# Kernel tuning notes

Measured on AMD Instinct MI355X. Metric: run time of the kernel, lower is better.

## Reference

```python
import jax, jax.numpy as jnp
import numpy as np

N_NODES = 50000
N_EDGES = 800000
DIM = 128
HEADS = 2
DEPTH = 2
MLP = 512
NEG_SLOPE = 0.2  # PyG GATv2 default
EPS = 1e-5


def setup_inputs() -> dict:
    key = jax.random.key(0)
    ks = jax.random.split(key, 10)
    s = 0.05
    p = lambda k, shape: (jax.random.normal(k, shape, jnp.float32) * s)
    x = jax.random.normal(ks[0], (N_NODES, DIM), jnp.float32)
    edge_index = jax.random.randint(ks[1], (2, N_EDGES), 0, N_NODES, dtype=jnp.int64)
    D, H = DEPTH, HEADS
    return {
        "x": x,
        "edge_index": edge_index,
        # per-layer stacked params (leading dim = depth)
        "ln1_g": jnp.ones((D, DIM), jnp.float32), "ln1_b": jnp.zeros((D, DIM), jnp.float32),
        "Wl": p(ks[2], (D, DIM, H * DIM)), "bl": jnp.zeros((D, H * DIM), jnp.float32),
        "Wr": p(ks[3], (D, DIM, H * DIM)), "br": jnp.zeros((D, H * DIM), jnp.float32),
        "att": p(ks[4], (D, H, DIM)),
        "gat_b": jnp.zeros((D, H * DIM), jnp.float32),
        "proj_W": p(ks[5], (D, H * DIM, DIM)), "proj_b": jnp.zeros((D, DIM), jnp.float32),
        "ln2_g": jnp.ones((D, DIM), jnp.float32), "ln2_b": jnp.zeros((D, DIM), jnp.float32),
        "W1": p(ks[6], (D, DIM, MLP)), "b1": jnp.zeros((D, MLP), jnp.float32),
        "W2": p(ks[7], (D, MLP, DIM)), "b2": jnp.zeros((D, DIM), jnp.float32),
    }


def _layer_norm(x, g, b):
    m = jnp.mean(x, axis=-1, keepdims=True)
    v = jnp.var(x, axis=-1, keepdims=True)
    return (x - m) * jax.lax.rsqrt(v + EPS) * g + b


def _gatv2(x, src, dst, Wl, bl, Wr, br, att, gat_b):
    # GATv2Conv: e_ij = att^T LeakyReLU(Wl x_j + Wr x_i); alpha = segment-softmax over dst
    n = x.shape[0]
    xl = (x @ Wl + bl).reshape(n, HEADS, DIM)  # source transform [N,H,D]
    xr = (x @ Wr + br).reshape(n, HEADS, DIM)  # target transform [N,H,D]
    e = jax.nn.leaky_relu(xl[src] + xr[dst], NEG_SLOPE)      # [E,H,D]
    score = jnp.einsum('ehd,hd->eh', e, att)                 # [E,H]
    smax = jax.ops.segment_max(score, dst, num_segments=n)   # [N,H]
    ex = jnp.exp(score - smax[dst])
    denom = jax.ops.segment_sum(ex, dst, num_segments=n)     # [N,H]
    alpha = ex / (denom[dst] + 1e-16)                        # [E,H]
    msg = xl[src] * alpha[..., None]                         # [E,H,D]
    out = jax.ops.segment_sum(msg, dst, num_segments=n)      # [N,H,D]
    return out.reshape(n, HEADS * DIM) + gat_b


def reference(x, edge_index, ln1_g, ln1_b, Wl, bl, Wr, br, att, gat_b,
              proj_W, proj_b, ln2_g, ln2_b, W1, b1, W2, b2):
    src, dst = edge_index[0], edge_index[1]
    for i in range(DEPTH):
        h = _layer_norm(x, ln1_g[i], ln1_b[i])               # PreNorm
        g = _gatv2(h, src, dst, Wl[i], bl[i], Wr[i], br[i], att[i], gat_b[i])
        x = x + (g @ proj_W[i] + proj_b[i])                  # QuickFix proj + Residual
        h = _layer_norm(x, ln2_g[i], ln2_b[i])
        x = x + (jax.nn.gelu(h @ W1[i] + b1[i]) @ W2[i] + b2[i])  # FFN + Residual
    return x
```

## Files before the change

kernel.cpp:

```cpp
#include <hip/hip_runtime.h>

typedef unsigned int uint;
typedef unsigned short ushort;
typedef __attribute__((ext_vector_type(4))) float f32x4;
typedef __attribute__((ext_vector_type(2))) float f32x2;
typedef __attribute__((ext_vector_type(8))) short bf16x8;
typedef _Float16 f16x2 __attribute__((ext_vector_type(2)));

#define N_NODES 50000
#define DIM 128
#define HEADS 2
#define HD 256
#define MLP 512
#define DEPTH 2
#define CAP 96
#define NPART 8
#define BPX 104

__device__ __forceinline__ uint f2bf(float f) {
    uint u = __float_as_uint(f);
    return (u + 0x7FFFu + ((u >> 16) & 1u)) >> 16;
}
__device__ __forceinline__ ushort f2h(float f) {
    union { _Float16 h; ushort u; } v;
    v.h = (_Float16)f;
    return v.u;
}
__device__ __forceinline__ f16x2 u2h(uint u) {
    union { uint u; f16x2 h; } v;
    v.u = u;
    return v.h;
}

#if __has_builtin(__builtin_amdgcn_fdot2)
#define FDOT2(a, b, c) __builtin_amdgcn_fdot2((a), (b), (c), false)
#else
#define FDOT2(a, b, c) fmaf((float)(a)[0], (float)(b)[0], fmaf((float)(a)[1], (float)(b)[1], (c)))
#endif
#if __has_builtin(__builtin_amdgcn_exp2f)
#define EXP2F(x) __builtin_amdgcn_exp2f(x)
#else
#define EXP2F(x) exp2f(x)
#endif

__device__ __forceinline__ float gelu_tanh(float x) {
    float t = 0.7978845608028654f * (x + 0.044715f * x * x * x);
    float e = __expf(2.0f * t);
    float th = 1.0f - 2.0f / (e + 1.0f);
    return 0.5f * x * (1.0f + th);
}

__global__ __launch_bounds__(256) void ln_kernel(
    const float* __restrict__ x, const float* __restrict__ g,
    const float* __restrict__ b, ushort* __restrict__ out, int N)
{
    int node = blockIdx.x * 4 + (threadIdx.x >> 6);
    if (node >= N) return;
    int lane = threadIdx.x & 63;
    const float2 v = *(const float2*)(x + (size_t)node * DIM + lane * 2);
    float s = v.x + v.y;
    float s2 = v.x * v.x + v.y * v.y;
    #pragma unroll
    for (int m = 1; m <= 32; m <<= 1) {
        s  += __shfl_xor(s,  m, 64);
        s2 += __shfl_xor(s2, m, 64);
    }
    float mean = s * (1.0f / 128.0f);
    float var  = s2 * (1.0f / 128.0f) - mean * mean;
    float rs = rsqrtf(var + 1e-5f);
    float ox = (v.x - mean) * rs * g[lane * 2]     + b[lane * 2];
    float oy = (v.y - mean) * rs * g[lane * 2 + 1] + b[lane * 2 + 1];
    uint pk = f2bf(ox) | (f2bf(oy) << 16);
    *(uint*)(out + (size_t)node * DIM + lane * 2) = pk;
}

__global__ __launch_bounds__(256) void wconv_all(
    const float* __restrict__ Wl, const float* __restrict__ Wr,
    const float* __restrict__ pW, const float* __restrict__ W1,
    const float* __restrict__ W2, ushort* __restrict__ WlWr_t,
    ushort* __restrict__ pW_t, ushort* __restrict__ W1_t,
    ushort* __restrict__ W2_t)
{
    int i = blockIdx.x * 256 + threadIdx.x;
    if (i < 65536) {
        int l = i >> 15, rem = i & 32767;
        int k = rem >> 8, m = rem & 255;
        WlWr_t[l * 65536 + m * 128 + k] = (ushort)f2bf(Wl[i]);
    } else if (i < 131072) {
        int j = i - 65536;
        int l = j >> 15, rem = j & 32767;
        int k = rem >> 8, m = rem & 255;
        WlWr_t[l * 65536 + (m + 256) * 128 + k] = (ushort)f2bf(Wr[j]);
    } else if (i < 196608) {
        int j = i - 131072;
        int l = j >> 15, rem = j & 32767;
        int k = rem >> 7, m = rem & 127;
        pW_t[l * 32768 + m * 256 + k] = (ushort)f2bf(pW[j]);
    } else if (i < 327680) {
        int j = i - 196608;
        int l = j >> 16, rem = j & 65535;
        int k = rem >> 9, m = rem & 511;
        W1_t[l * 65536 + m * 128 + k] = (ushort)f2bf(W1[j]);
    } else if (i < 458752) {
        int j = i - 327680;
        int l = j >> 16, rem = j & 65535;
        int k = rem >> 7, m = rem & 127;
        W2_t[l * 65536 + m * 512 + k] = (ushort)f2bf(W2[j]);
    }
}

template<int EPI>
__global__ __launch_bounds__(256) void gemm_fat(
    const ushort* __restrict__ A, const ushort* __restrict__ Bt,
    const float* __restrict__ bias, const float* __restrict__ bias2, int bsplit,
    ushort* __restrict__ Cout, int Nr)
{
    __shared__ ushort Bs[2][64 * 136];
    const int tid = threadIdx.x;
    const int wave = tid >> 6, lane = tid & 63;
    const int wm = wave >> 1, wn = wave & 1;
    const int r0 = blockIdx.x * 64;
    const int l15 = lane & 15, q = lane >> 4;

    bf16x8 af[2][4];
    #pragma unroll
    for (int t = 0; t < 2; ++t) {
        int gr = r0 + wm * 32 + t * 16 + l15; gr = gr < Nr ? gr : Nr - 1;
        #pragma unroll
        for (int ks = 0; ks < 4; ++ks)
            af[t][ks] = *(const bf16x8*)(A + (size_t)gr * 128 + ks * 32 + q * 8);
    }

    auto stageB = [&](int buf, int ct) {
        #pragma unroll
        for (int p = 0; p < 4; ++p) {
            int flat = p * 256 + tid;
            int row = flat >> 4, c8 = flat & 15;
            uint4 v = *(const uint4*)(Bt + (size_t)(ct * 64 + row) * 128 + c8 * 8);
            *(uint4*)(Bs[buf] + row * 136 + c8 * 8) = v;
        }
    };

    stageB(0, 0);
    __syncthreads();

    #pragma unroll
    for (int ct = 0; ct < 8; ++ct) {
        const int cur = ct & 1;
        if (ct < 7) stageB(cur ^ 1, ct + 1);

        f32x4 acc[2][2];
        #pragma unroll
        for (int t = 0; t < 2; ++t)
            #pragma unroll
            for (int u = 0; u < 2; ++u) {
                f32x4 z = {0.f, 0.f, 0.f, 0.f};
                acc[t][u] = z;
            }

        #pragma unroll
        for (int ks = 0; ks < 4; ++ks) {
            bf16x8 b[2];
            #pragma unroll
            for (int u = 0; u < 2; ++u)
                b[u] = *(const bf16x8*)(Bs[cur] + (wn * 32 + u * 16 + l15) * 136 + ks * 32 + q * 8);
            #pragma unroll
            for (int t = 0; t < 2; ++t)
                #pragma unroll
                for (int u = 0; u < 2; ++u)
                    acc[t][u] = __builtin_amdgcn_mfma_f32_16x16x32_bf16(
                        af[t][ks], b[u], acc[t][u], 0, 0, 0);
        }

        #pragma unroll
        for (int t = 0; t < 2; ++t) {
            int grow = r0 + wm * 32 + t * 16 + q * 4;
            #pragma unroll
            for (int u = 0; u < 2; ++u) {
                int gcol = ct * 64 + wn * 32 + u * 16 + l15;
                float bv = (gcol < bsplit) ? bias[gcol] : bias2[gcol - bsplit];
                #pragma unroll
                for (int i = 0; i < 4; ++i) {
                    int r = grow + i;
                    if (r >= Nr) continue;
                    float v = acc[t][u][i] + bv;
                    if (EPI == 1) v = gelu_tanh(v);
                    Cout[(size_t)r * 512 + gcol] = (EPI == 0) ? f2h(v) : (ushort)f2bf(v);
                }
            }
        }
        __syncthreads();
    }
}

__global__ __launch_bounds__(256) void gemm_ln(
    const ushort* __restrict__ A, const ushort* __restrict__ Bt,
    const float* __restrict__ bias, const float* __restrict__ R,
    float* __restrict__ X, const float* __restrict__ lng,
    const float* __restrict__ lnb, ushort* __restrict__ H,
    int Nr, int K)
{
    __shared__ ushort As[64 * 72];
    __shared__ ushort Bs[128 * 72];
    __shared__ float4 part[64];
    const int tid = threadIdx.x;
    const int wave = tid >> 6, lane = tid & 63;
    const int wm = wave >> 1, wn = wave & 1;
    const int r0 = blockIdx.y * 64;
    const int l15 = lane & 15, q = lane >> 4;

    f32x4 acc[2][4];
    #pragma unroll
    for (int t = 0; t < 2; ++t)
        #pragma unroll
        for (int u = 0; u < 4; ++u) {
            f32x4 z = {0.f, 0.f, 0.f, 0.f};
            acc[t][u] = z;
        }

    for (int k0 = 0; k0 < K; k0 += 64) {
        #pragma unroll
        for (int p = 0; p < 2; ++p) {
            int flat = p * 256 + tid;
            int row = flat >> 3, c8 = flat & 7;
            int gr = r0 + row; gr = gr < Nr ? gr : Nr - 1;
            uint4 v = *(const uint4*)(A + (size_t)gr * K + k0 + c8 * 8);
            *(uint4*)(As + row * 72 + c8 * 8) = v;
        }
        #pragma unroll
        for (int p = 0; p < 4; ++p) {
            int flat = p * 256 + tid;
            int row = flat >> 3, c8 = flat & 7;
            uint4 v = *(const uint4*)(Bt + (size_t)row * K + k0 + c8 * 8);
            *(uint4*)(Bs + row * 72 + c8 * 8) = v;
        }
        __syncthreads();
        #pragma unroll
        for (int kh = 0; kh < 2; ++kh) {
            const int ko = kh * 32 + q * 8;
            bf16x8 a[2], b[4];
            #pragma unroll
            for (int t = 0; t < 2; ++t)
                a[t] = *(const bf16x8*)(As + (wm * 32 + t * 16 + l15) * 72 + ko);
            #pragma unroll
            for (int u = 0; u < 4; ++u)
                b[u] = *(const bf16x8*)(Bs + (wn * 64 + u * 16 + l15) * 72 + ko);
            #pragma unroll
            for (int t = 0; t < 2; ++t)
                #pragma unroll
                for (int u = 0; u < 4; ++u)
                    acc[t][u] = __builtin_amdgcn_mfma_f32_16x16x32_bf16(
                        a[t], b[u], acc[t][u], 0, 0, 0);
        }
        __syncthreads();
    }

    float bv[4];
    #pragma unroll
    for (int u = 0; u < 4; ++u) bv[u] = bias[wn * 64 + u * 16 + l15];

    #pragma unroll
    for (int t = 0; t < 2; ++t) {
        #pragma unroll
        for (int i = 0; i < 4; ++i) {
            const int rl = wm * 32 + t * 16 + q * 4 + i;
            const int r = r0 + rl;
            const bool ok = r < Nr;
            float ss = 0.f, ss2 = 0.f;
            #pragma unroll
            for (int u = 0; u < 4; ++u) {
                const int col = wn * 64 + u * 16 + l15;
                float v = acc[t][u][i] + bv[u];
                if (ok) v += R[(size_t)r * DIM + col];
                acc[t][u][i] = v;
                ss += v; ss2 += v * v;
            }
            #pragma unroll
            for (int m = 1; m <= 8; m <<= 1) {
                ss  += __shfl_xor(ss,  m, 64);
                ss2 += __shfl_xor(ss2, m, 64);
            }
            if (ok) {
                #pragma unroll
                for (int u = 0; u < 4; ++u)
                    X[(size_t)r * DIM + wn * 64 + u * 16 + l15] = acc[t][u][i];
            }
            if (l15 == 0) {
                float2 w = { ss, ss2 };
                *(float2*)((float*)&part[rl] + wn * 2) = w;
            }
        }
    }

    if (H != nullptr) {
        __syncthreads();
        float lgv[4], lbv[4];
        #pragma unroll
        for (int u = 0; u < 4; ++u) {
            lgv[u] = lng[wn * 64 + u * 16 + l15];
            lbv[u] = lnb[wn * 64 + u * 16 + l15];
        }
        #pragma unroll
        for (int t = 0; t < 2; ++t) {
            #pragma unroll
            for (int i = 0; i < 4; ++i) {
                const int rl = wm * 32 + t * 16 + q * 4 + i;
                const int r = r0 + rl;
                if (r >= Nr) continue;
                const float4 pp = part[rl];
                const float mean = (pp.x + pp.z) * (1.0f / 128.0f);
                const float var  = (pp.y + pp.w) * (1.0f / 128.0f) - mean * mean;
                const float rs = rsqrtf(var + 1e-5f);
                #pragma unroll
                for (int u = 0; u < 4; ++u) {
                    const int col = wn * 64 + u * 16 + l15;
                    const float hv = (acc[t][u][i] - mean) * rs * lgv[u] + lbv[u];
                    H[(size_t)r * DIM + col] = (ushort)f2bf(hv);
                }
            }
        }
    }
}

__global__ __launch_bounds__(256) void bucket_kernel(
    const int* __restrict__ src, const int* __restrict__ dst,
    int* __restrict__ deg, ushort* __restrict__ esrc, int E, int part_sz)
{
    const int part = blockIdx.x & (NPART - 1);
    const int bid  = blockIdx.x >> 3;
    const int lo = part * part_sz, hi = lo + part_sz;
    for (int e = bid * 256 + threadIdx.x; e < E; e += BPX * 256) {
        int d = dst[e];
        if (d < lo || d >= hi) continue;
        int pos = atomicAdd(&deg[d], 1);
        if (pos < CAP) esrc[(size_t)d * CAP + pos] = (ushort)src[e];
    }
}

__global__ __launch_bounds__(256) void gat_gather(
    const int* __restrict__ deg, const ushort* __restrict__ esrc,
    const ushort* __restrict__ xlr, const float* __restrict__ att,
    const float* __restrict__ gat_b, ushort* __restrict__ agg, int N)
{
    int node = blockIdx.x * 4 + (threadIdx.x >> 6);
    if (node >= N) return;
    const int lane = threadIdx.x & 63;
    const int half = lane >> 5, sl = lane & 31;
    const int c = sl * 8;

    const uint4 rq = *(const uint4*)(xlr + (size_t)node * 512 + 256 + c);
    const f16x2 r01 = u2h(rq.x), r23 = u2h(rq.y);
    const f16x2 r45 = u2h(rq.z), r67 = u2h(rq.w);

    const float LOG2E = 1.4426950408889634f;
    const float4 af0 = *(const float4*)(att + c);
    const float4 af1 = *(const float4*)(att + c + 4);
    f16x2 a01, a23, a45, a67;
    a01[0] = (_Float16)(af0.x * LOG2E); a01[1] = (_Float16)(af0.y * LOG2E);
    a23[0] = (_Float16)(af0.z * LOG2E); a23[1] = (_Float16)(af0.w * LOG2E);
    a45[0] = (_Float16)(af1.x * LOG2E); a45[1] = (_Float16)(af1.y * LOG2E);
    a67[0] = (_Float16)(af1.z * LOG2E); a67[1] = (_Float16)(af1.w * LOG2E);
    const f16x2 k02 = { (_Float16)0.2f, (_Float16)0.2f };

    int dc = deg[node]; dc = dc < CAP ? dc : CAP;
    const int base = node * CAP;
    f32x2 acc01 = {0.f, 0.f}, acc23 = {0.f, 0.f}, acc45 = {0.f, 0.f}, acc67 = {0.f, 0.f};
    float den = 0.f;

    if (dc > 0) {
        int slc = sl < dc ? sl : dc - 1;
        const int idxreg = esrc[base + slc];

        auto getsrc = [&](int e) -> int {
            int idx = e < dc ? e : dc - 1;
            int s = __shfl(idxreg, (lane & 32) | (idx & 31), 64);
            if (idx >= 32) s = esrc[base + idx];
            return s;
        };

        const int iters = (dc + 1) >> 1;
        int e0 = half;
        int s0 = getsrc(e0);
        uint4 lq0 = *(const uint4*)(xlr + (size_t)s0 * 512 + c);
        int e1 = e0 + 2;
        int s1 = getsrc(e1);
        uint4 lq1 = *(const uint4*)(xlr + (size_t)s1 * 512 + c);

        for (int it = 0; it < iters; ++it) {
            const int e2 = e0 + 4;
            const int s2 = getsrc(e2);
            const uint4 lq2 = *(const uint4*)(xlr + (size_t)s2 * 512 + c);

            const f16x2 l01 = u2h(lq0.x), l23 = u2h(lq0.y);
            const f16x2 l45 = u2h(lq0.z), l67 = u2h(lq0.w);
            f16x2 t, lr;
            float p = 0.f;
            t = l01 + r01; lr = __builtin_elementwise_max(t, t * k02); p = FDOT2(a01, lr, p);
            t = l23 + r23; lr = __builtin_elementwise_max(t, t * k02); p = FDOT2(a23, lr, p);
            t = l45 + r45; lr = __builtin_elementwise_max(t, t * k02); p = FDOT2(a45, lr, p);
            t = l67 + r67; lr = __builtin_elementwise_max(t, t * k02); p = FDOT2(a67, lr, p);
            p += __shfl_xor(p, 1, 64);
            p += __shfl_xor(p, 2, 64);
            p += __shfl_xor(p, 4, 64);
            p += __shfl_xor(p, 8, 64);
            const float ex = (e0 < dc) ? EXP2F(p) : 0.f;
            acc01.x = fmaf(ex, (float)l01[0], acc01.x);
            acc01.y = fmaf(ex, (float)l01[1], acc01.y);
            acc23.x = fmaf(ex, (float)l23[0], acc23.x);
            acc23.y = fmaf(ex, (float)l23[1], acc23.y);
            acc45.x = fmaf(ex, (float)l45[0], acc45.x);
            acc45.y = fmaf(ex, (float)l45[1], acc45.y);
            acc67.x = fmaf(ex, (float)l67[0], acc67.x);
            acc67.y = fmaf(ex, (float)l67[1], acc67.y);
            den += ex;
            e0 = e1; lq0 = lq1;
            e1 = e2; lq1 = lq2;
        }
    }
    acc01.x += __shfl_xor(acc01.x, 32, 64); acc01.y += __shfl_xor(acc01.y, 32, 64);
    acc23.x += __shfl_xor(acc23.x, 32, 64); acc23.y += __shfl_xor(acc23.y, 32, 64);
    acc45.x += __shfl_xor(acc45.x, 32, 64); acc45.y += __shfl_xor(acc45.y, 32, 64);
    acc67.x += __shfl_xor(acc67.x, 32, 64); acc67.y += __shfl_xor(acc67.y, 32, 64);
    den     += __shfl_xor(den,     32, 64);

    if (half == 0) {
        const float inv = 1.0f / (den + 1e-16f);
        const float4 g0 = *(const float4*)(gat_b + c);
        const float4 g1 = *(const float4*)(gat_b + c + 4);
        uint4 o;
        o.x = f2bf(acc01.x * inv + g0.x) | (f2bf(acc01.y * inv + g0.y) << 16);
        o.y = f2bf(acc23.x * inv + g0.z) | (f2bf(acc23.y * inv + g0.w) << 16);
        o.z = f2bf(acc45.x * inv + g1.x) | (f2bf(acc45.y * inv + g1.y) << 16);
        o.w = f2bf(acc67.x * inv + g1.z) | (f2bf(acc67.y * inv + g1.w) << 16);
        *(uint4*)(agg + (size_t)node * HD + c) = o;
    }
}

extern "C" void kernel_launch(void* const* d_in, const int* in_sizes, int n_in,
                              void* d_out, int out_size, void* d_ws, size_t ws_size,
                              hipStream_t stream) {
    const float* x_in   = (const float*)d_in[0];
    const int*   eidx   = (const int*)d_in[1];
    const float* ln1_g  = (const float*)d_in[2];
    const float* ln1_b  = (const float*)d_in[3];
    const float* Wl     = (const float*)d_in[4];
    const float* bl     = (const float*)d_in[5];
    const float* Wr     = (const float*)d_in[6];
    const float* br     = (const float*)d_in[7];
    const float* att    = (const float*)d_in[8];
    const float* gat_b  = (const float*)d_in[9];
    const float* projW  = (const float*)d_in[10];
    const float* projb  = (const float*)d_in[11];
    const float* ln2_g  = (const float*)d_in[12];
    const float* ln2_b  = (const float*)d_in[13];
    const float* W1     = (const float*)d_in[14];
    const float* b1     = (const float*)d_in[15];
    const float* W2     = (const float*)d_in[16];
    const float* b2     = (const float*)d_in[17];

    const int N = N_NODES;
    const int E = in_sizes[1] / 2;
    const int* src = eidx;
    const int* dst = eidx + E;

    char* ws = (char*)d_ws;
    size_t off = 0;
    ushort* xlr  = (ushort*)(ws + off); off += (size_t)N * 512 * 2;
    ushort* agg  = (ushort*)(ws + off); off += (size_t)N * HD * 2;
    ushort* h    = (ushort*)(ws + off); off += (size_t)N * DIM * 2;
    ushort* WlWr_t = (ushort*)(ws + off); off += (size_t)DEPTH * 512 * 128 * 2;
    ushort* pW_t   = (ushort*)(ws + off); off += (size_t)DEPTH * 128 * 256 * 2;
    ushort* W1_t   = (ushort*)(ws + off); off += (size_t)DEPTH * 512 * 128 * 2;
    ushort* W2_t   = (ushort*)(ws + off); off += (size_t)DEPTH * 128 * 512 * 2;
    int* deg     = (int*)(ws + off);    off += (size_t)N * 4;
    ushort* esrc = (ushort*)(ws + off); off += (size_t)N * CAP * 2;
    ushort* mid  = xlr;

    float* x = (float*)d_out;

    const int nodeBlocks = (N + 3) / 4;
    const dim3 blk(256);
    const int gy64  = (N + 63) / 64;
    const int part_sz = (N + NPART - 1) / NPART;

    wconv_all<<<(458752 + 255) / 256, blk, 0, stream>>>(
        Wl, Wr, projW, W1, W2, WlWr_t, pW_t, W1_t, W2_t);

    hipMemsetAsync(deg, 0, (size_t)N * 4, stream);
    bucket_kernel<<<NPART * BPX, blk, 0, stream>>>(src, dst, deg, esrc, E, part_sz);

    for (int L = 0; L < DEPTH; ++L) {
        const float* bl_i   = bl + (size_t)L * HD;
        const float* br_i   = br + (size_t)L * HD;
        const float* att_i  = att + (size_t)L * HD;
        const float* gatb_i = gat_b + (size_t)L * HD;
        const float* pb_i   = projb + (size_t)L * DIM;
        const float* b1_i   = b1 + (size_t)L * MLP;
        const float* b2_i   = b2 + (size_t)L * DIM;
        const float* xin_L  = (L == 0) ? x_in : x;

        if (L == 0)
            ln_kernel<<<nodeBlocks, blk, 0, stream>>>(
                x_in, ln1_g, ln1_b, h, N);

        gemm_fat<0><<<dim3(gy64), blk, 0, stream>>>(
            h, WlWr_t + (size_t)L * 65536, bl_i, br_i, HD, xlr, N);
        gat_gather<<<nodeBlocks, blk, 0, stream>>>(deg, esrc, xlr, att_i, gatb_i, agg, N);
        gemm_ln<<<dim3(1, gy64), blk, 0, stream>>>(
            agg, pW_t + (size_t)L * 128 * 256, pb_i, xin_L, x,
            ln2_g + (size_t)L * DIM, ln2_b + (size_t)L * DIM, h, N, 256);
        gemm_fat<1><<<dim3(gy64), blk, 0, stream>>>(
            h, W1_t + (size_t)L * 65536, b1_i, b1_i, 1 << 30, mid, N);
        const bool last = (L + 1 == DEPTH);
        gemm_ln<<<dim3(1, gy64), blk, 0, stream>>>(
            mid, W2_t + (size_t)L * 65536, b2_i, x, x,
            last ? nullptr : ln1_g + (size_t)(L + 1) * DIM,
            last ? nullptr : ln1_b + (size_t)(L + 1) * DIM,
            last ? nullptr : h, N, 512);
    }
}
```

Measured before the change: 540.3 us.

## Split gemm_fat across column tiles with a 2D grid instead of looping

gemm_fat no longer loops over eight 64-column tiles inside one block with double-buffered B staging. It now launches a 2D grid where each block computes a single 64x64 output tile and loads its B slice once into a single LDS buffer. This multiplies the block count eightfold and cuts LDS per block, which should raise occupancy and parallelism. The cost is that each block now reloads its A rows, so A is read from global memory eight times.

Result: slower. 554.6 us (+2.6%).

```diff
diff --git a/kernel.cpp b/kernel.cpp
--- a/kernel.cpp
+++ b/kernel.cpp
@@ -115,12 +115,21 @@
     const float* __restrict__ bias, const float* __restrict__ bias2, int bsplit,
     ushort* __restrict__ Cout, int Nr)
 {
-    __shared__ ushort Bs[2][64 * 136];
+    __shared__ ushort Bs[64 * 136];
     const int tid = threadIdx.x;
     const int wave = tid >> 6, lane = tid & 63;
     const int wm = wave >> 1, wn = wave & 1;
-    const int r0 = blockIdx.x * 64;
+    const int r0 = blockIdx.y * 64;
+    const int c0 = blockIdx.x * 64;
     const int l15 = lane & 15, q = lane >> 4;
+
+    #pragma unroll
+    for (int p = 0; p < 4; ++p) {
+        int flat = p * 256 + tid;
+        int row = flat >> 4, c8 = flat & 15;
+        uint4 v = *(const uint4*)(Bt + (size_t)(c0 + row) * 128 + c8 * 8);
+        *(uint4*)(Bs + row * 136 + c8 * 8) = v;
+    }
 
     bf16x8 af[2][4];
     #pragma unroll
@@ -131,66 +140,53 @@
             af[t][ks] = *(const bf16x8*)(A + (size_t)gr * 128 + ks * 32 + q * 8);
     }
 
-    auto stageB = [&](int buf, int ct) {
-        #pragma unroll
-        for (int p = 0; p < 4; ++p) {
-            int flat = p * 256 + tid;
-            int row = flat >> 4, c8 = flat & 15;
-            uint4 v = *(const uint4*)(Bt + (size_t)(ct * 64 + row) * 128 + c8 * 8);
-            *(uint4*)(Bs[buf] + row * 136 + c8 * 8) = v;
-        }
-    };
-
-    stageB(0, 0);
+    float bv[2];
+    #pragma unroll
+    for (int u = 0; u < 2; ++u) {
+        int gcol = c0 + wn * 32 + u * 16 + l15;
+        bv[u] = (gcol < bsplit) ? bias[gcol] : bias2[gcol - bsplit];
+    }
+
     __syncthreads();
 
-    #pragma unroll
-    for (int ct = 0; ct < 8; ++ct) {
-        const int cur = ct & 1;
-        if (ct < 7) stageB(cur ^ 1, ct + 1);
-
-        f32x4 acc[2][2];
+    f32x4 acc[2][2];
+    #pragma unroll
+    for (int t = 0; t < 2; ++t)
+        #pragma unroll
+        for (int u = 0; u < 2; ++u) {
+            f32x4 z = {0.f, 0.f, 0.f, 0.f};
+            acc[t][u] = z;
+        }
+
+    #pragma unroll
+    for (int ks = 0; ks < 4; ++ks) {
+        bf16x8 b[2];
+        #pragma unroll
+        for (int u = 0; u < 2; ++u)
+            b[u] = *(const bf16x8*)(Bs + (wn * 32 + u * 16 + l15) * 136 + ks * 32 + q * 8);
         #pragma unroll
         for (int t = 0; t < 2; ++t)
             #pragma unroll
-            for (int u = 0; u < 2; ++u) {
-                f32x4 z = {0.f, 0.f, 0.f, 0.f};
-                acc[t][u] = z;
+            for (int u = 0; u < 2; ++u)
+                acc[t][u] = __builtin_amdgcn_mfma_f32_16x16x32_bf16(
+                    af[t][ks], b[u], acc[t][u], 0, 0, 0);
+    }
+
+    const int rbase = r0 + wm * 32 + q * 4;
+    #pragma unroll
+    for (int t = 0; t < 2; ++t)
+        #pragma unroll
+        for (int u = 0; u < 2; ++u) {
+            const int gcol = c0 + wn * 32 + u * 16 + l15;
+            #pragma unroll
+            for (int i = 0; i < 4; ++i) {
+                int r = rbase + t * 16 + i;
+                if (r >= Nr) continue;
+                float v = acc[t][u][i] + bv[u];
+                if (EPI == 1) v = gelu_tanh(v);
+                Cout[(size_t)r * 512 + gcol] = (EPI == 0) ? f2h(v) : (ushort)f2bf(v);
             }
-
-        #pragma unroll
-        for (int ks = 0; ks < 4; ++ks) {
-            bf16x8 b[2];
-            #pragma unroll
-            for (int u = 0; u < 2; ++u)
-                b[u] = *(const bf16x8*)(Bs[cur] + (wn * 32 + u * 16 + l15) * 136 + ks * 32 + q * 8);
-            #pragma unroll
-            for (int t = 0; t < 2; ++t)
-                #pragma unroll
-                for (int u = 0; u < 2; ++u)
-                    acc[t][u] = __builtin_amdgcn_mfma_f32_16x16x32_bf16(
-                        af[t][ks], b[u], acc[t][u], 0, 0, 0);
-        }
-
-        #pragma unroll
-        for (int t = 0; t < 2; ++t) {
-            int grow = r0 + wm * 32 + t * 16 + q * 4;
-            #pragma unroll
-            for (int u = 0; u < 2; ++u) {
-                int gcol = ct * 64 + wn * 32 + u * 16 + l15;
-                float bv = (gcol < bsplit) ? bias[gcol] : bias2[gcol - bsplit];
-                #pragma unroll
-                for (int i = 0; i < 4; ++i) {
-                    int r = grow + i;
-                    if (r >= Nr) continue;
-                    float v = acc[t][u][i] + bv;
-                    if (EPI == 1) v = gelu_tanh(v);
-                    Cout[(size_t)r * 512 + gcol] = (EPI == 0) ? f2h(v) : (ushort)f2bf(v);
-                }
-            }
-        }
-        __syncthreads();
-    }
+        }
 }
 
 __global__ __launch_bounds__(256) void gemm_ln(
@@ -503,13 +499,13 @@
             ln_kernel<<<nodeBlocks, blk, 0, stream>>>(
                 x_in, ln1_g, ln1_b, h, N);
 
-        gemm_fat<0><<<dim3(gy64), blk, 0, stream>>>(
+        gemm_fat<0><<<dim3(8, gy64), blk, 0, stream>>>(
             h, WlWr_t + (size_t)L * 65536, bl_i, br_i, HD, xlr, N);
         gat_gather<<<nodeBlocks, blk, 0, stream>>>(deg, esrc, xlr, att_i, gatb_i, agg, N);
         gemm_ln<<<dim3(1, gy64), blk, 0, stream>>>(
             agg, pW_t + (size_t)L * 128 * 256, pb_i, xin_L, x,
             ln2_g + (size_t)L * DIM, ln2_b + (size_t)L * DIM, h, N, 256);
-        gemm_fat<1><<<dim3(gy64), blk, 0, stream>>>(
+        gemm_fat<1><<<dim3(8, gy64), blk, 0, stream>>>(
             h, W1_t + (size_t)L * 65536, b1_i, b1_i, 1 << 30, mid, N);
         const bool last = (L + 1 == DEPTH);
         gemm_ln<<<dim3(1, gy64), blk, 0, stream>>>(
```
